# Kernel tuning notes

Hardware: AMD Instinct MI355X
Metric: run time of the kernel (lower is better)

The kernel has to match this reference:

```python
import jax, jax.numpy as jnp
import numpy as np

OUT_H = 7
OUT_W = 7
C = 256
SPATIAL_SCALE = 0.0625
SAMPLING_RATIO = 2
GAMMA = 0.1
SIGMA = 0.5
FDIM = OUT_H * OUT_W * C  # 12544
DFC = 1024
B, H, W = 4, 100, 152
N_ROIS = 512
IMG_H, IMG_W = H / SPATIAL_SCALE, W / SPATIAL_SCALE


def _bilinear(feat, b, y, x):
    # feat: [B,H,W,C]; b int32 and y,x float coords, mutually broadcastable.
    Hf, Wf = feat.shape[1], feat.shape[2]
    valid = (y > -1.0) & (y < Hf) & (x > -1.0) & (x < Wf)
    yc = jnp.clip(y, 0.0, Hf - 1.0)
    xc = jnp.clip(x, 0.0, Wf - 1.0)
    y0 = jnp.clip(jnp.floor(yc).astype(jnp.int32), 0, Hf - 2)
    x0 = jnp.clip(jnp.floor(xc).astype(jnp.int32), 0, Wf - 2)
    ly = yc - y0.astype(yc.dtype)
    lx = xc - x0.astype(xc.dtype)
    hy, hx = 1.0 - ly, 1.0 - lx
    val = ((hy * hx)[..., None] * feat[b, y0, x0]
           + (hy * lx)[..., None] * feat[b, y0, x0 + 1]
           + (ly * hx)[..., None] * feat[b, y0 + 1, x0]
           + (ly * lx)[..., None] * feat[b, y0 + 1, x0 + 1])
    return jnp.where(valid[..., None], val, jnp.zeros((), val.dtype))


def deform_roi_pool(inp, rois, offset):
    # mmcv DeformRoIPool semantics; rois get no gradient (torch returns None).
    rois = jax.lax.stop_gradient(rois)
    feat = jnp.transpose(inp, (0, 2, 3, 1))  # [B,H,W,C]
    n = rois.shape[0]
    b = rois[:, 0].astype(jnp.int32)[:, None, None, None, None]
    x1 = rois[:, 1] * SPATIAL_SCALE - 0.5
    y1 = rois[:, 2] * SPATIAL_SCALE - 0.5
    x2 = rois[:, 3] * SPATIAL_SCALE - 0.5
    y2 = rois[:, 4] * SPATIAL_SCALE - 0.5
    rw, rh = x2 - x1, y2 - y1
    bw, bh = rw / OUT_W, rh / OUT_H
    start_w = jnp.broadcast_to(x1[:, None, None], (n, OUT_H, OUT_W))
    start_h = jnp.broadcast_to(y1[:, None, None], (n, OUT_H, OUT_W))
    if offset is not None:
        start_w = start_w + GAMMA * rw[:, None, None] * offset[:, 0]
        start_h = start_h + GAMMA * rh[:, None, None] * offset[:, 1]
    g = (jnp.arange(SAMPLING_RATIO, dtype=inp.dtype) + 0.5) / SAMPLING_RATIO
    ph = jnp.arange(OUT_H, dtype=inp.dtype)
    pw = jnp.arange(OUT_W, dtype=inp.dtype)
    # per-bin sample coords: ys,xs -> [n,oh,ow,g]
    ys = start_h[..., None] + (ph[None, :, None, None] + g) * bh[:, None, None, None]
    xs = start_w[..., None] + (pw[None, None, :, None] + g) * bw[:, None, None, None]
    yy = ys[..., :, None]  # [n,oh,ow,g,1]
    xx = xs[..., None, :]  # [n,oh,ow,1,g]
    val = _bilinear(feat, b, yy, xx)  # [n,oh,ow,g,g,C]
    out = val.mean(axis=(3, 4))  # count = g*g samples per bin
    return jnp.transpose(out, (0, 3, 1, 2))  # [n,C,oh,ow]


def _make_rois(key, n):
    k1, k2, k3, k4, k5 = jax.random.split(key, 5)
    bi = jax.random.randint(k1, (n,), 0, B).astype(jnp.float32)
    cx = jax.random.uniform(k2, (n,)) * IMG_W
    cy = jax.random.uniform(k3, (n,)) * IMG_H
    w = 32.0 + jax.random.uniform(k4, (n,)) * 300.0
    h = 32.0 + jax.random.uniform(k5, (n,)) * 300.0
    x1 = jnp.clip(cx - 0.5 * w, 0.0, IMG_W - 1.0)
    x2 = jnp.clip(cx + 0.5 * w, 0.0, IMG_W - 1.0)
    y1 = jnp.clip(cy - 0.5 * h, 0.0, IMG_H - 1.0)
    y2 = jnp.clip(cy + 0.5 * h, 0.0, IMG_H - 1.0)
    return jnp.stack([bi, x1, y1, x2, y2], axis=1)


def setup_inputs() -> dict:
    key = jax.random.key(0)
    ks = jax.random.split(key, 12)
    inp = jax.random.normal(ks[0], (B, C, H, W), dtype=jnp.float32)
    rois = _make_rois(ks[1], N_ROIS)
    s = 0.02
    return {
        'input': inp,
        'rois': rois,
        'rescale_w': s * jax.random.normal(ks[2], (OUT_H * OUT_W * 2, FDIM), jnp.float32),
        'rescale_b': s * jax.random.normal(ks[3], (OUT_H * OUT_W * 2,), jnp.float32),
        'off_w1': s * jax.random.normal(ks[4], (DFC, FDIM), jnp.float32),
        'off_b1': s * jax.random.normal(ks[5], (DFC,), jnp.float32),
        'off_w2': s * jax.random.normal(ks[6], (DFC, DFC), jnp.float32),
        'off_b2': s * jax.random.normal(ks[7], (DFC,), jnp.float32),
        'off_w3': s * jax.random.normal(ks[8], (OUT_H * OUT_W * 2, DFC), jnp.float32),
        'off_b3': s * jax.random.normal(ks[9], (OUT_H * OUT_W * 2,), jnp.float32),
    }


def reference(input, rois, rescale_w, rescale_b, off_w1, off_b1, off_w2, off_b2, off_w3, off_b3):
    x_cls = deform_roi_pool(input, rois, None)  # [N,C,7,7]
    n = rois.shape[0]
    flat = x_cls.reshape(n, -1)  # torch .view(N,-1) on NCHW layout
    rescale = 1.0 + SIGMA * jax.nn.sigmoid(flat @ rescale_w.T + rescale_b)
    # rescale_roi uses only columns 0..3 of the rescale head output
    cx = (rois[:, 1] + rois[:, 3]) * 0.5 + rescale[:, 0]
    cy = (rois[:, 2] + rois[:, 4]) * 0.5 + rescale[:, 1]
    nw = (rois[:, 3] - rois[:, 1]) * rescale[:, 2]
    nh = (rois[:, 4] - rois[:, 2]) * rescale[:, 3]
    new_rois = jnp.stack([rois[:, 0], cx - 0.5 * nw, cy - 0.5 * nh,
                          cx + 0.5 * nw, cy + 0.5 * nh], axis=-1)
    h1 = jax.nn.relu(flat @ off_w1.T + off_b1)
    h2 = jax.nn.relu(h1 @ off_w2.T + off_b2)
    off = (h2 @ off_w3.T + off_b3).reshape(n, 2, OUT_H, OUT_W)
    x_reg = deform_roi_pool(input, new_rois, off)
    return x_cls, x_reg
```

## Files before the change

### kernel.cpp

```cpp
#include <hip/hip_runtime.h>
#include <math.h>

#define NCH 256
#define HH 100
#define WW 152
#define BB 4
#define NROIS 512
#define FDIM 12544
#define DFC 1024
#define HW 15200

typedef unsigned short u16;
typedef float f32x2 __attribute__((ext_vector_type(2)));
typedef float f32x4 __attribute__((ext_vector_type(4)));
typedef short s16x8 __attribute__((ext_vector_type(8)));
typedef __bf16 bf16x8 __attribute__((ext_vector_type(8)));

template<int WITH_OFF>
__global__ __launch_bounds__(256) void pool_nchw(
    const float* __restrict__ feat, const float* __restrict__ rois,
    const float* __restrict__ offp, float* __restrict__ out) {
  const int n    = blockIdx.x;
  const int tid  = threadIdx.x;
  const int wave = tid >> 6;
  const int lane = tid & 63;
  float r[5];
  const float* rp = rois + n * 5;
  #pragma unroll
  for (int i = 0; i < 5; ++i) r[i] = rp[i];
  int b = (int)r[0];
  b = min(max(b, 0), BB - 1);
  const float x1 = r[1] * 0.0625f - 0.5f;
  const float y1 = r[2] * 0.0625f - 0.5f;
  const float x2 = r[3] * 0.0625f - 0.5f;
  const float y2 = r[4] * 0.0625f - 0.5f;
  const float rw = x2 - x1, rh = y2 - y1;
  const float bw = rw * (1.0f / 7.0f), bh = rh * (1.0f / 7.0f);
  const int bin = lane;
  const bool active = (bin < 49);
  const int ph = bin / 7;
  const int pw = bin - ph * 7;
  float sw = x1, sh = y1;
  if (WITH_OFF && active) {
    sw += 0.1f * rw * offp[n * 98 + bin];
    sh += 0.1f * rh * offp[n * 98 + 49 + bin];
  }
  int idx[4];
  float wt[4][4];
  bool val[4];
  #pragma unroll
  for (int s = 0; s < 4; ++s) {
    const int i = s >> 1, j = s & 1;
    const float y = sh + ((float)ph + 0.25f + 0.5f * (float)i) * bh;
    const float x = sw + ((float)pw + 0.25f + 0.5f * (float)j) * bw;
    val[s] = active && (y > -1.0f) && (y < (float)HH) && (x > -1.0f) && (x < (float)WW);
    float yc = fminf(fmaxf(y, 0.f), (float)(HH - 1));
    float xc = fminf(fmaxf(x, 0.f), (float)(WW - 1));
    int y0 = min(max((int)floorf(yc), 0), HH - 2);
    int x0 = min(max((int)floorf(xc), 0), WW - 2);
    const float ly = yc - (float)y0, lx = xc - (float)x0;
    const float hy = 1.f - ly, hx = 1.f - lx;
    idx[s] = y0 * WW + x0;
    wt[s][0] = hy * hx; wt[s][1] = hy * lx;
    wt[s][2] = ly * hx; wt[s][3] = ly * lx;
  }
  const float* fb = feat + (size_t)b * NCH * HW;
  float* op = out + (size_t)n * FDIM;
  for (int c = wave; c < NCH; c += 4) {
    const float* plane = fb + (size_t)c * HW;
    float acc = 0.f;
    #pragma unroll
    for (int s = 0; s < 4; ++s) {
      if (val[s]) {
        const float* p = plane + idx[s];
        acc += wt[s][0] * p[0] + wt[s][1] * p[1]
             + wt[s][2] * p[WW] + wt[s][3] * p[WW + 1];
      }
    }
    if (active) op[c * 49 + bin] = acc * 0.25f;
  }
}

__global__ __launch_bounds__(256) void nchw_to_nhwc(
    const float* __restrict__ in, float* __restrict__ outp) {
  __shared__ float tile[64][65];
  const int b  = blockIdx.z;
  const int c0 = blockIdx.y * 64;
  const int p0 = blockIdx.x * 64;
  const int tx = threadIdx.x & 63;
  const int ty = threadIdx.x >> 6;
  const float* ib = in + ((size_t)b * NCH + c0) * HW + p0;
  #pragma unroll
  for (int i = 0; i < 16; ++i) {
    const int r = ty + i * 4;
    tile[r][tx] = (p0 + tx < HW) ? ib[(size_t)r * HW + tx] : 0.f;
  }
  __syncthreads();
  float* ob = outp + ((size_t)b * HW + p0) * NCH + c0;
  #pragma unroll
  for (int i = 0; i < 16; ++i) {
    const int pr = ty + i * 4;
    if (p0 + pr < HW) ob[(size_t)pr * NCH + tx] = tile[tx][pr];
  }
}

template<int WITH_OFF>
__global__ __launch_bounds__(256) void pool_nhwc_cg(
    const float* __restrict__ feat, const float* __restrict__ rois,
    const float* __restrict__ offp, float* __restrict__ out) {
  __shared__ float obuf[64 * 49];
  const int n  = blockIdx.x;
  const int cg = blockIdx.y;
  const int w    = threadIdx.x >> 6;
  const int lane = threadIdx.x & 63;
  const int c = cg * 64 + lane;
  float r[5];
  const float* rp = rois + n * 5;
  #pragma unroll
  for (int i = 0; i < 5; ++i) r[i] = rp[i];
  int b = (int)r[0];
  b = min(max(b, 0), BB - 1);
  const float x1 = r[1] * 0.0625f - 0.5f;
  const float y1 = r[2] * 0.0625f - 0.5f;
  const float x2 = r[3] * 0.0625f - 0.5f;
  const float y2 = r[4] * 0.0625f - 0.5f;
  const float rw = x2 - x1, rh = y2 - y1;
  const float bw = rw * (1.0f / 7.0f), bh = rh * (1.0f / 7.0f);
  const float* fb = feat + (size_t)b * HW * NCH + c;
  for (int bin = w; bin < 49; bin += 4) {
    const int ph = bin / 7;
    const int pw = bin - ph * 7;
    float sw = x1, sh = y1;
    if (WITH_OFF) {
      sw += 0.1f * rw * offp[n * 98 + bin];
      sh += 0.1f * rh * offp[n * 98 + 49 + bin];
    }
    float acc = 0.f;
    #pragma unroll
    for (int s = 0; s < 4; ++s) {
      const int i = s >> 1, j = s & 1;
      const float y = sh + ((float)ph + 0.25f + 0.5f * (float)i) * bh;
      const float x = sw + ((float)pw + 0.25f + 0.5f * (float)j) * bw;
      const bool val = (y > -1.0f) && (y < (float)HH) && (x > -1.0f) && (x < (float)WW);
      float yc = fminf(fmaxf(y, 0.f), (float)(HH - 1));
      float xc = fminf(fmaxf(x, 0.f), (float)(WW - 1));
      int y0 = min(max((int)floorf(yc), 0), HH - 2);
      int x0 = min(max((int)floorf(xc), 0), WW - 2);
      const float ly = yc - (float)y0, lx = xc - (float)x0;
      const float hy = 1.f - ly, hx = 1.f - lx;
      if (val) {
        const float* p = fb + ((size_t)y0 * WW + x0) * NCH;
        acc += (hy * hx) * p[0] + (hy * lx) * p[NCH]
             + (ly * hx) * p[WW * NCH] + (ly * lx) * p[WW * NCH + NCH];
      }
    }
    obuf[lane * 49 + bin] = acc * 0.25f;
  }
  __syncthreads();
  float* op = out + (size_t)n * FDIM + cg * 64 * 49;
  for (int i = threadIdx.x; i < 64 * 49; i += 256) op[i] = obuf[i];
}

__global__ __launch_bounds__(256) void rescale_rois_kernel(
    const float* __restrict__ flat, const float* __restrict__ w,
    const float* __restrict__ bsc, const float* __restrict__ rois,
    float* __restrict__ new_rois) {
  __shared__ float red[4];
  const int n = blockIdx.x;
  const int j = threadIdx.x >> 6;
  const int lane = threadIdx.x & 63;
  const float* a = flat + (size_t)n * FDIM;
  const float* wj = w + (size_t)j * FDIM;
  float acc = 0.f;
  for (int k = lane * 8; k + 8 <= FDIM; k += 64 * 8) {
    f32x4 a0 = *(const f32x4*)(a + k);
    f32x4 a1 = *(const f32x4*)(a + k + 4);
    f32x4 w0 = *(const f32x4*)(wj + k);
    f32x4 w1 = *(const f32x4*)(wj + k + 4);
    float s = 0.f;
    #pragma unroll
    for (int e = 0; e < 4; ++e) s += a0[e] * w0[e];
    #pragma unroll
    for (int e = 0; e < 4; ++e) s += a1[e] * w1[e];
    acc += s;
  }
  #pragma unroll
  for (int d = 32; d > 0; d >>= 1)
    acc += __shfl_down(acc, d, 64);
  if (lane == 0) red[j] = acc;
  __syncthreads();
  if (threadIdx.x == 0) {
    float rr[5];
    const float* rp = rois + n * 5;
    #pragma unroll
    for (int i = 0; i < 5; ++i) rr[i] = rp[i];
    float sc[4];
    #pragma unroll
    for (int jj = 0; jj < 4; ++jj) {
      const float z = red[jj] + bsc[jj];
      sc[jj] = 1.0f + 0.5f / (1.0f + expf(-z));
    }
    const float cx = (rr[1] + rr[3]) * 0.5f + sc[0];
    const float cy = (rr[2] + rr[4]) * 0.5f + sc[1];
    const float nw = (rr[3] - rr[1]) * sc[2];
    const float nh = (rr[4] - rr[2]) * sc[3];
    float* o = new_rois + n * 5;
    o[0] = rr[0];
    o[1] = cx - 0.5f * nw;
    o[2] = cy - 0.5f * nh;
    o[3] = cx + 0.5f * nw;
    o[4] = cy + 0.5f * nh;
  }
}

__global__ __launch_bounds__(512, 4) void gemm_mfma_sk(
    const float* __restrict__ A, const float* __restrict__ B,
    float* __restrict__ part, int M, int N, int Ns, int K, int kchunk) {
  __shared__ __align__(16) u16 Ah[64 * 32];
  __shared__ __align__(16) u16 Al[64 * 32];
  __shared__ __align__(16) u16 Bh[128 * 32];
  __shared__ __align__(16) u16 Bl[128 * 32];
  const int tid  = threadIdx.x;
  const int wave = tid >> 6;
  const int lane = tid & 63;
  const int q  = lane >> 4;
  const int rr = lane & 15;
  const int wr = wave >> 2;
  const int wc = wave & 3;
  const int m0 = blockIdx.y * 64;
  const int n0 = blockIdx.x * 128;
  const int s  = blockIdx.z;
  const int kb = s * kchunk, ke = kb + kchunk;

  const int srow  = tid >> 2;
  const int sslot = tid & 3;
  const int swz   = sslot ^ ((srow >> 1) & 3);
  const bool astage = tid < 256;
  u16* const a_sth = &Ah[srow * 32 + swz * 8];
  u16* const a_stl = &Al[srow * 32 + swz * 8];
  u16* const b_sth = &Bh[srow * 32 + swz * 8];
  u16* const b_stl = &Bl[srow * 32 + swz * 8];
  const float* Ap = A + (size_t)(m0 + (astage ? srow : 0)) * K + sslot * 8;
  const int  brow = n0 + srow;
  const bool bok  = brow < N;
  const float* Bp = B + (size_t)(bok ? brow : 0) * K + sslot * 8;

  const int rsw = q ^ ((rr >> 1) & 3);
  const u16* const a_rdh = &Ah[(wr * 32 + rr) * 32 + rsw * 8];
  const u16* const a_rdl = &Al[(wr * 32 + rr) * 32 + rsw * 8];
  const u16* const b_rdh = &Bh[(wc * 32 + rr) * 32 + rsw * 8];
  const u16* const b_rdl = &Bl[(wc * 32 + rr) * 32 + rsw * 8];

  f32x4 acc[2][2];
  #pragma unroll
  for (int mt = 0; mt < 2; ++mt)
    #pragma unroll
    for (int nt = 0; nt < 2; ++nt) acc[mt][nt] = (f32x4){0.f, 0.f, 0.f, 0.f};

  for (int k0 = kb; k0 < ke; k0 += 32) {
    f32x4 a0 = (f32x4){0.f, 0.f, 0.f, 0.f}, a1 = a0, b0 = a0, b1 = a0;
    if (astage) { a0 = *(const f32x4*)(Ap + k0); a1 = *(const f32x4*)(Ap + k0 + 4); }
    if (bok)    { b0 = *(const f32x4*)(Bp + k0); b1 = *(const f32x4*)(Bp + k0 + 4); }
    bf16x8 avh, avl, bvh, bvl;
    #pragma unroll
    for (int e = 0; e < 4; ++e) {
      const __bf16 h0 = (__bf16)a0[e], h1 = (__bf16)a1[e];
      avh[e] = h0; avh[e + 4] = h1;
      avl[e]     = (__bf16)(a0[e] - (float)h0);
      avl[e + 4] = (__bf16)(a1[e] - (float)h1);
      const __bf16 g0 = (__bf16)b0[e], g1 = (__bf16)b1[e];
      bvh[e] = g0; bvh[e + 4] = g1;
      bvl[e]     = (__bf16)(b0[e] - (float)g0);
      bvl[e + 4] = (__bf16)(b1[e] - (float)g1);
    }
    __syncthreads();
    if (astage) { *(bf16x8*)a_sth = avh; *(bf16x8*)a_stl = avl; }
    *(bf16x8*)b_sth = bvh;
    *(bf16x8*)b_stl = bvl;
    __syncthreads();
    bf16x8 ah[2], al[2], bh[2], bl[2];
    #pragma unroll
    for (int mt = 0; mt < 2; ++mt) {
      ah[mt] = *(const bf16x8*)(a_rdh + mt * 16 * 32);
      al[mt] = *(const bf16x8*)(a_rdl + mt * 16 * 32);
    }
    #pragma unroll
    for (int nt = 0; nt < 2; ++nt) {
      bh[nt] = *(const bf16x8*)(b_rdh + nt * 16 * 32);
      bl[nt] = *(const bf16x8*)(b_rdl + nt * 16 * 32);
    }
    #pragma unroll
    for (int mt = 0; mt < 2; ++mt)
      #pragma unroll
      for (int nt = 0; nt < 2; ++nt) {
        acc[mt][nt] = __builtin_amdgcn_mfma_f32_16x16x32_bf16(ah[mt], bh[nt], acc[mt][nt], 0, 0, 0);
        acc[mt][nt] = __builtin_amdgcn_mfma_f32_16x16x32_bf16(al[mt], bh[nt], acc[mt][nt], 0, 0, 0);
        acc[mt][nt] = __builtin_amdgcn_mfma_f32_16x16x32_bf16(ah[mt], bl[nt], acc[mt][nt], 0, 0, 0);
      }
  }

  float* pb = part + (size_t)s * M * Ns;
  #pragma unroll
  for (int mt = 0; mt < 2; ++mt)
    #pragma unroll
    for (int nt = 0; nt < 2; ++nt) {
      const int col = n0 + wc * 32 + nt * 16 + rr;
      #pragma unroll
      for (int i = 0; i < 4; ++i) {
        const int row = m0 + wr * 32 + mt * 16 + q * 4 + i;
        pb[(size_t)row * Ns + col] = acc[mt][nt][i];
      }
    }
}

template<int RELU>
__global__ __launch_bounds__(256) void reduce_sk(
    const float* __restrict__ part, const float* __restrict__ bias,
    float* __restrict__ out, int M, int N, int Ns, int S) {
  const int idx = blockIdx.x * 256 + threadIdx.x;
  if (idx >= M * Ns) return;
  const int m = idx / Ns, n = idx - m * Ns;
  if (n >= N) return;
  float v = bias[n];
  for (int s = 0; s < S; ++s) v += part[(size_t)s * M * Ns + idx];
  if (RELU) v = fmaxf(v, 0.f);
  out[(size_t)m * N + n] = v;
}

extern "C" void kernel_launch(void* const* d_in, const int* in_sizes, int n_in,
                              void* d_out, int out_size, void* d_ws, size_t ws_size,
                              hipStream_t stream) {
  const float* input  = (const float*)d_in[0];
  const float* rois   = (const float*)d_in[1];
  const float* resc_w = (const float*)d_in[2];
  const float* resc_b = (const float*)d_in[3];
  const float* w1     = (const float*)d_in[4];
  const float* b1     = (const float*)d_in[5];
  const float* w2     = (const float*)d_in[6];
  const float* b2     = (const float*)d_in[7];
  const float* w3     = (const float*)d_in[8];
  const float* b3     = (const float*)d_in[9];
  float* out = (float*)d_out;

  char* ws = (char*)d_ws;
  float* part   = (float*)ws;
  float* h1     = (float*)(ws + (16u << 20));
  float* h2     = (float*)(ws + (18u << 20));
  float* offbuf = (float*)(ws + (22u << 20));
  float* nrois  = (float*)(ws + (22u << 20) + 256 * 1024);
  float* feat_t = (float*)(ws + ((size_t)24 << 20));
  const size_t feat_t_bytes = (size_t)BB * HW * NCH * sizeof(float);
  const bool big = ws_size >= (((size_t)24 << 20) + feat_t_bytes);

  float* x_cls = out;
  float* x_reg = out + (size_t)NROIS * FDIM;

  if (big) {
    nchw_to_nhwc<<<dim3(238, 4, 4), 256, 0, stream>>>(input, feat_t);
    pool_nhwc_cg<0><<<dim3(NROIS, 4), 256, 0, stream>>>(feat_t, rois, nullptr, x_cls);
  } else {
    pool_nchw<0><<<NROIS, 256, 0, stream>>>(input, rois, nullptr, x_cls);
  }
  rescale_rois_kernel<<<NROIS, 256, 0, stream>>>(x_cls, resc_w, resc_b, rois, nrois);

  gemm_mfma_sk<<<dim3(8, 8, 8), 512, 0, stream>>>(x_cls, w1, part, NROIS, DFC, DFC, FDIM, FDIM / 8);
  reduce_sk<1><<<(NROIS * DFC + 255) / 256, 256, 0, stream>>>(part, b1, h1, NROIS, DFC, DFC, 8);
  gemm_mfma_sk<<<dim3(8, 8, 8), 512, 0, stream>>>(h1, w2, part, NROIS, DFC, DFC, DFC, DFC / 8);
  reduce_sk<1><<<(NROIS * DFC + 255) / 256, 256, 0, stream>>>(part, b2, h2, NROIS, DFC, DFC, 8);
  gemm_mfma_sk<<<dim3(1, 8, 8), 512, 0, stream>>>(h2, w3, part, NROIS, 98, 128, DFC, DFC / 8);
  reduce_sk<0><<<(NROIS * 128 + 255) / 256, 256, 0, stream>>>(part, b3, offbuf, NROIS, 98, 128, 8);

  if (big) pool_nhwc_cg<1><<<dim3(NROIS, 4), 256, 0, stream>>>(feat_t, nrois, offbuf, x_reg);
  else     pool_nchw<1><<<NROIS, 256, 0, stream>>>(input, nrois, offbuf, x_reg);
}
```

Measured before the change: 342.7 us.

## Pre-split GEMM activations into bf16 hi/lo pairs at producer kernels

The pooling kernel and the split-K reducers now also write each activation as a pair of bf16 values, a high part and a low-residual part. A new GEMM kernel loads these pre-split pairs directly, so it no longer converts fp32 A tiles to bf16 inside the K loop. It still splits B on the fly and runs three MFMAs per tile pair for near-fp32 accuracy. In exchange the code adds extra global writes of the split arrays and needs a much larger workspace, and it only takes this path when the workspace is big enough.

```diff
diff --git a/kernel.cpp b/kernel.cpp
--- a/kernel.cpp
+++ b/kernel.cpp
@@ -15,6 +15,16 @@
 typedef float f32x4 __attribute__((ext_vector_type(4)));
 typedef short s16x8 __attribute__((ext_vector_type(8)));
 typedef __bf16 bf16x8 __attribute__((ext_vector_type(8)));
+
+__device__ __forceinline__ u16 f2bf(float f) {
+  union { float f; unsigned u; } c; c.f = f;
+  unsigned u = c.u;
+  return (u16)((u + 0x7FFFu + ((u >> 16) & 1u)) >> 16);
+}
+__device__ __forceinline__ float bf2f(u16 h) {
+  union { unsigned u; float f; } c; c.u = ((unsigned)h) << 16;
+  return c.f;
+}
 
 template<int WITH_OFF>
 __global__ __launch_bounds__(256) void pool_nchw(
@@ -104,10 +114,11 @@
   }
 }
 
-template<int WITH_OFF>
+template<int WITH_OFF, int SPLIT>
 __global__ __launch_bounds__(256) void pool_nhwc_cg(
     const float* __restrict__ feat, const float* __restrict__ rois,
-    const float* __restrict__ offp, float* __restrict__ out) {
+    const float* __restrict__ offp, float* __restrict__ out,
+    u16* __restrict__ ahi, u16* __restrict__ alo) {
   __shared__ float obuf[64 * 49];
   const int n  = blockIdx.x;
   const int cg = blockIdx.y;
@@ -157,8 +168,17 @@
     obuf[lane * 49 + bin] = acc * 0.25f;
   }
   __syncthreads();
-  float* op = out + (size_t)n * FDIM + cg * 64 * 49;
-  for (int i = threadIdx.x; i < 64 * 49; i += 256) op[i] = obuf[i];
+  const size_t base = (size_t)n * FDIM + (size_t)cg * (64 * 49);
+  float* op = out + base;
+  for (int i = threadIdx.x; i < 64 * 49; i += 256) {
+    const float v = obuf[i];
+    op[i] = v;
+    if (SPLIT) {
+      const u16 h = f2bf(v);
+      ahi[base + i] = h;
+      alo[base + i] = f2bf(v - bf2f(h));
+    }
+  }
 }
 
 __global__ __launch_bounds__(256) void rescale_rois_kernel(
@@ -313,6 +333,131 @@
     }
 }
 
+__global__ __launch_bounds__(512) void gemm_mfma_ps_sk(
+    const u16* __restrict__ Ahi, const u16* __restrict__ Alo,
+    const float* __restrict__ B,
+    float* __restrict__ part, int M, int N, int Ns, int K, int kchunk) {
+  __shared__ __align__(16) u16 AhB[2][64 * 32];
+  __shared__ __align__(16) u16 AlB[2][64 * 32];
+  __shared__ __align__(16) u16 BhB[2][128 * 32];
+  __shared__ __align__(16) u16 BlB[2][128 * 32];
+  const int tid  = threadIdx.x;
+  const int wave = tid >> 6;
+  const int lane = tid & 63;
+  const int q  = lane >> 4;
+  const int rr = lane & 15;
+  const int wr = wave >> 2;
+  const int wc = wave & 3;
+  const int m0 = blockIdx.y * 64;
+  const int n0 = blockIdx.x * 128;
+  const int s  = blockIdx.z;
+  const int kb = s * kchunk, ke = kb + kchunk;
+
+  const int srow  = tid >> 2;
+  const int sslot = tid & 3;
+  const int swz   = sslot ^ ((srow >> 1) & 3);
+  const bool astage = tid < 256;
+  const int ast = srow * 32 + swz * 8;
+  const u16* Aph = Ahi + (size_t)(m0 + (astage ? srow : 0)) * K + sslot * 8;
+  const u16* Apl = Alo + (size_t)(m0 + (astage ? srow : 0)) * K + sslot * 8;
+  const int  brow = n0 + srow;
+  const bool bok  = brow < N;
+  const float* Bp = B + (size_t)(bok ? brow : 0) * K + sslot * 8;
+
+  const int rsw = q ^ ((rr >> 1) & 3);
+  const int ard = (wr * 32 + rr) * 32 + rsw * 8;
+  const int brd = (wc * 32 + rr) * 32 + rsw * 8;
+
+  f32x4 acc[2][2];
+  #pragma unroll
+  for (int mt = 0; mt < 2; ++mt)
+    #pragma unroll
+    for (int nt = 0; nt < 2; ++nt) acc[mt][nt] = (f32x4){0.f, 0.f, 0.f, 0.f};
+
+  {
+    s16x8 avh, avl;
+    f32x4 b0 = (f32x4){0.f, 0.f, 0.f, 0.f}, b1 = b0;
+    if (astage) { avh = *(const s16x8*)(Aph + kb); avl = *(const s16x8*)(Apl + kb); }
+    if (bok)    { b0 = *(const f32x4*)(Bp + kb); b1 = *(const f32x4*)(Bp + kb + 4); }
+    bf16x8 bvh, bvl;
+    #pragma unroll
+    for (int e = 0; e < 4; ++e) {
+      const __bf16 g0 = (__bf16)b0[e], g1 = (__bf16)b1[e];
+      bvh[e] = g0; bvh[e + 4] = g1;
+      bvl[e]     = (__bf16)(b0[e] - (float)g0);
+      bvl[e + 4] = (__bf16)(b1[e] - (float)g1);
+    }
+    if (astage) { *(s16x8*)&AhB[0][ast] = avh; *(s16x8*)&AlB[0][ast] = avl; }
+    *(bf16x8*)&BhB[0][ast] = bvh;
+    *(bf16x8*)&BlB[0][ast] = bvl;
+  }
+  __syncthreads();
+
+  int cur = 0;
+  for (int k0 = kb; k0 < ke; k0 += 32) {
+    const bool nx = (k0 + 32 < ke);
+    s16x8 navh, navl;
+    f32x4 nb0 = (f32x4){0.f, 0.f, 0.f, 0.f}, nb1 = nb0;
+    if (nx) {
+      if (astage) {
+        navh = *(const s16x8*)(Aph + k0 + 32);
+        navl = *(const s16x8*)(Apl + k0 + 32);
+      }
+      if (bok) {
+        nb0 = *(const f32x4*)(Bp + k0 + 32);
+        nb1 = *(const f32x4*)(Bp + k0 + 36);
+      }
+    }
+    bf16x8 ah[2], al[2], bh2[2], bl2[2];
+    #pragma unroll
+    for (int mt = 0; mt < 2; ++mt) {
+      ah[mt] = *(const bf16x8*)&AhB[cur][ard + mt * 16 * 32];
+      al[mt] = *(const bf16x8*)&AlB[cur][ard + mt * 16 * 32];
+    }
+    #pragma unroll
+    for (int nt = 0; nt < 2; ++nt) {
+      bh2[nt] = *(const bf16x8*)&BhB[cur][brd + nt * 16 * 32];
+      bl2[nt] = *(const bf16x8*)&BlB[cur][brd + nt * 16 * 32];
+    }
+    #pragma unroll
+    for (int mt = 0; mt < 2; ++mt)
+      #pragma unroll
+      for (int nt = 0; nt < 2; ++nt) {
+        acc[mt][nt] = __builtin_amdgcn_mfma_f32_16x16x32_bf16(ah[mt], bh2[nt], acc[mt][nt], 0, 0, 0);
+        acc[mt][nt] = __builtin_amdgcn_mfma_f32_16x16x32_bf16(al[mt], bh2[nt], acc[mt][nt], 0, 0, 0);
+        acc[mt][nt] = __builtin_amdgcn_mfma_f32_16x16x32_bf16(ah[mt], bl2[nt], acc[mt][nt], 0, 0, 0);
+      }
+    if (nx) {
+      bf16x8 nbvh, nbvl;
+      #pragma unroll
+      for (int e = 0; e < 4; ++e) {
+        const __bf16 g0 = (__bf16)nb0[e], g1 = (__bf16)nb1[e];
+        nbvh[e] = g0; nbvh[e + 4] = g1;
+        nbvl[e]     = (__bf16)(nb0[e] - (float)g0);
+        nbvl[e + 4] = (__bf16)(nb1[e] - (float)g1);
+      }
+      if (astage) { *(s16x8*)&AhB[cur ^ 1][ast] = navh; *(s16x8*)&AlB[cur ^ 1][ast] = navl; }
+      *(bf16x8*)&BhB[cur ^ 1][ast] = nbvh;
+      *(bf16x8*)&BlB[cur ^ 1][ast] = nbvl;
+    }
+    __syncthreads();
+    cur ^= 1;
+  }
+
+  float* pb = part + (size_t)s * M * Ns;
+  #pragma unroll
+  for (int mt = 0; mt < 2; ++mt)
+    #pragma unroll
+    for (int nt = 0; nt < 2; ++nt) {
+      const int col = n0 + wc * 32 + nt * 16 + rr;
+      #pragma unroll
+      for (int i = 0; i < 4; ++i) {
+        const int row = m0 + wr * 32 + mt * 16 + q * 4 + i;
+        pb[(size_t)row * Ns + col] = acc[mt][nt][i];
+      }
+    }
+}
+
 template<int RELU>
 __global__ __launch_bounds__(256) void reduce_sk(
     const float* __restrict__ part, const float* __restrict__ bias,
@@ -325,6 +470,20 @@
   for (int s = 0; s < S; ++s) v += part[(size_t)s * M * Ns + idx];
   if (RELU) v = fmaxf(v, 0.f);
   out[(size_t)m * N + n] = v;
+}
+
+__global__ __launch_bounds__(256) void reduce_sk_split(
+    const float* __restrict__ part, const float* __restrict__ bias,
+    u16* __restrict__ oh, u16* __restrict__ ol, int M, int N, int S) {
+  const int idx = blockIdx.x * 256 + threadIdx.x;
+  if (idx >= M * N) return;
+  const int n = idx % N;
+  float v = bias[n];
+  for (int s = 0; s < S; ++s) v += part[(size_t)s * M * N + idx];
+  v = fmaxf(v, 0.f);
+  const u16 h = f2bf(v);
+  oh[idx] = h;
+  ol[idx] = f2bf(v - bf2f(h));
 }
 
 extern "C" void kernel_launch(void* const* d_in, const int* in_sizes, int n_in,
@@ -343,33 +502,65 @@
   float* out = (float*)d_out;
 
   char* ws = (char*)d_ws;
-  float* part   = (float*)ws;
+  const size_t feat_t_bytes = (size_t)BB * HW * NCH * sizeof(float);
+
+  float* part    = (float*)ws;
+  u16*   h1h     = (u16*)(ws + (16u << 20));
+  u16*   h1l     = (u16*)(ws + (17u << 20));
+  u16*   h2h     = (u16*)(ws + (18u << 20));
+  u16*   h2l     = (u16*)(ws + (19u << 20));
+  float* offbuf2 = (float*)(ws + (20u << 20));
+  float* nrois2  = (float*)(ws + (20u << 20) + 512 * 1024);
+  u16*   Ahi     = (u16*)(ws + (21u << 20));
+  u16*   Alo     = (u16*)(ws + (34u << 20));
+  float* feat_t2 = (float*)(ws + (47u << 20));
+  const bool big2 = ws_size >= ((size_t)(47u << 20) + feat_t_bytes);
+
   float* h1     = (float*)(ws + (16u << 20));
   float* h2     = (float*)(ws + (18u << 20));
   float* offbuf = (float*)(ws + (22u << 20));
   float* nrois  = (float*)(ws + (22u << 20) + 256 * 1024);
   float* feat_t = (float*)(ws + ((size_t)24 << 20));
-  const size_t feat_t_bytes = (size_t)BB * HW * NCH * sizeof(float);
   const bool big = ws_size >= (((size_t)24 << 20) + feat_t_bytes);
 
   float* x_cls = out;
   float* x_reg = out + (size_t)NROIS * FDIM;
 
-  if (big) {
+  if (big2) {
+    nchw_to_nhwc<<<dim3(238, 4, 4), 256, 0, stream>>>(input, feat_t2);
+    pool_nhwc_cg<0, 1><<<dim3(NROIS, 4), 256, 0, stream>>>(feat_t2, rois, nullptr, x_cls, Ahi, Alo);
+    rescale_rois_kernel<<<NROIS, 256, 0, stream>>>(x_cls, resc_w, resc_b, rois, nrois2);
+
+    gemm_mfma_ps_sk<<<dim3(8, 8, 8), 512, 0, stream>>>(Ahi, Alo, w1, part, NROIS, DFC, DFC, FDIM, FDIM / 8);
+    reduce_sk_split<<<(NROIS * DFC + 255) / 256, 256, 0, stream>>>(part, b1, h1h, h1l, NROIS, DFC, 8);
+    gemm_mfma_ps_sk<<<dim3(8, 8, 8), 512, 0, stream>>>(h1h, h1l, w2, part, NROIS, DFC, DFC, DFC, DFC / 8);
+    reduce_sk_split<<<(NROIS * DFC + 255) / 256, 256, 0, stream>>>(part, b2, h2h, h2l, NROIS, DFC, 8);
+    gemm_mfma_ps_sk<<<dim3(1, 8, 8), 512, 0, stream>>>(h2h, h2l, w3, part, NROIS, 98, 128, DFC, DFC / 8);
+    reduce_sk<0><<<(NROIS * 128 + 255) / 256, 256, 0, stream>>>(part, b3, offbuf2, NROIS, 98, 128, 8);
+
+    pool_nhwc_cg<1, 0><<<dim3(NROIS, 4), 256, 0, stream>>>(feat_t2, nrois2, offbuf2, x_reg, nullptr, nullptr);
+  } else if (big) {
     nchw_to_nhwc<<<dim3(238, 4, 4), 256, 0, stream>>>(input, feat_t);
-    pool_nhwc_cg<0><<<dim3(NROIS, 4), 256, 0, stream>>>(feat_t, rois, nullptr, x_cls);
+    pool_nhwc_cg<0, 0><<<dim3(NROIS, 4), 256, 0, stream>>>(feat_t, rois, nullptr, x_cls, nullptr, nullptr);
+    rescale_rois_kernel<<<NROIS, 256, 0, stream>>>(x_cls, resc_w, resc_b, rois, nrois);
+
+    gemm_mfma_sk<<<dim3(8, 8, 8), 512, 0, stream>>>(x_cls, w1, part, NROIS, DFC, DFC, FDIM, FDIM / 8);
+    reduce_sk<1><<<(NROIS * DFC + 255) / 256, 256, 0, stream>>>(part, b1, h1, NROIS, DFC, DFC, 8);
+    gemm_mfma_sk<<<dim3(8, 8, 8), 512, 0, stream>>>(h1, w2, part, NROIS, DFC, DFC, DFC, DFC / 8);
+    reduce_sk<1><<<(NROIS * DFC + 255) / 256, 256, 0, stream>>>(part, b2, h2, NROIS, DFC, DFC, 8);
+    gemm_mfma_sk<<<dim3(1, 8, 8), 512, 0, stream>>>(h2, w3, part, NROIS, 98, 128, DFC, DFC / 8);
+    reduce_sk<0><<<(NROIS * 128 + 255) / 256, 256, 0, stream>>>(part, b3, offbuf, NROIS, 98, 128, 8);
+
+    pool_nhwc_cg<1, 0><<<dim3(NROIS, 4), 256, 0, stream>>>(feat_t, nrois, offbuf, x_reg, nullptr, nullptr);
   } else {
     pool_nchw<0><<<NROIS, 256, 0, stream>>>(input, rois, nullptr, x_cls);
-  }
-  rescale_rois_kernel<<<NROIS, 256, 0, stream>>>(x_cls, resc_w, resc_b, rois, nrois);
-
-  gemm_mfma_sk<<<dim3(8, 8, 8), 512, 0, stream>>>(x_cls, w1, part, NROIS, DFC, DFC, FDIM, FDIM / 8);
-  reduce_sk<1><<<(NROIS * DFC + 255) / 256, 256, 0, stream>>>(part, b1, h1, NROIS, DFC, DFC, 8);
-  gemm_mfma_sk<<<dim3(8, 8, 8), 512, 0, stream>>>(h1, w2, part, NROIS, DFC, DFC, DFC, DFC / 8);
-  reduce_sk<1><<<(NROIS * DFC + 255) / 256, 256, 0, stream>>>(part, b2, h2, NROIS, DFC, DFC, 8);
-  gemm_mfma_sk<<<dim3(1, 8, 8), 512, 0, stream>>>(h2, w3, part, NROIS, 98, 128, DFC, DFC / 8);
-  reduce_sk<0><<<(NROIS * 128 + 255) / 256, 256, 0, stream>>>(part, b3, offbuf, NROIS, 98, 128, 8);
-
-  if (big) pool_nhwc_cg<1><<<dim3(NROIS, 4), 256, 0, stream>>>(feat_t, nrois, offbuf, x_reg);
-  else     pool_nchw<1><<<NROIS, 256, 0, stream>>>(input, nrois, offbuf, x_reg);
-}
+    rescale_rois_kernel<<<NROIS, 256, 0, stream>>>(x_cls, resc_w, resc_b, rois, nrois);
+    gemm_mfma_sk<<<dim3(8, 8, 8), 512, 0, stream>>>(x_cls, w1, part, NROIS, DFC, DFC, FDIM, FDIM / 8);
+    reduce_sk<1><<<(NROIS * DFC + 255) / 256, 256, 0, stream>>>(part, b1, h1, NROIS, DFC, DFC, 8);
+    gemm_mfma_sk<<<dim3(8, 8, 8), 512, 0, stream>>>(h1, w2, part, NROIS, DFC, DFC, DFC, DFC / 8);
+    reduce_sk<1><<<(NROIS * DFC + 255) / 256, 256, 0, stream>>>(part, b2, h2, NROIS, DFC, DFC, 8);
+    gemm_mfma_sk<<<dim3(1, 8, 8), 512, 0, stream>>>(h2, w3, part, NROIS, 98, 128, DFC, DFC / 8);
+    reduce_sk<0><<<(NROIS * 128 + 255) / 256, 256, 0, stream>>>(part, b3, offbuf, NROIS, 98, 128, 8);
+    pool_nchw<1><<<NROIS, 256, 0, stream>>>(input, nrois, offbuf, x_reg);
+  }
+}
```

After: 359.0 us. 1.05x slower.
